# Kernel optimization log

Hardware: AMD Instinct MI355X
Metric: run time of the kernel (lower is better)

The kernel has to match this reference:

```python
import jax, jax.numpy as jnp
import numpy as np

N_HEAD = 16
SPARSE_TOPK = 64
NEG_INF = float('-inf')


def setup_inputs() -> dict:
    key = jax.random.key(0)
    ks = jax.random.split(key, 12)
    B, T, C = 4, 1024, 1024
    s = 0.02
    q = jax.random.normal(ks[0], (B, T, C), jnp.float32)
    kv = jax.random.normal(ks[1], (B, T, C), jnp.float32)  # forward asserts k == v
    tgt_mask = jnp.tril(jnp.ones((T, T), jnp.bool_)).reshape(1, 1, T, T)
    inp = {'q': q, 'k': kv, 'v': kv, 'tgt_mask': tgt_mask}
    for i, n in enumerate(['Wq', 'Wk', 'Wv', 'Wo']):
        inp[n] = jax.random.normal(ks[2 + i], (C, C), jnp.float32) * s
    for i, n in enumerate(['bq', 'bk', 'bv', 'bo']):
        inp[n] = jax.random.normal(ks[6 + i], (C,), jnp.float32) * s
    return inp


def reference(q, k, v, tgt_mask, Wq, Wk, Wv, Wo, bq, bk, bv, bo):
    B, T, C = q.shape
    H = N_HEAD
    hd = C // H
    scale = 1.0 / np.sqrt(hd).astype(np.float32)
    # QKV projections -> [B, H, T, hd]
    qh = (q @ Wq + bq).reshape(B, T, H, hd).transpose(0, 2, 1, 3)
    kh = (k @ Wk + bk).reshape(B, T, H, hd).transpose(0, 2, 1, 3)
    vh = (v @ Wv + bv).reshape(B, T, H, hd).transpose(0, 2, 1, 3)
    # full attention scores [B, H, T, T]
    att = jnp.einsum('bhtd,bhsd->bhts', qh, kh) * scale
    # causal mask: masked_fill where tgt_mask == 0
    att = jnp.where(tgt_mask[:, :, :T, :T], att, NEG_INF)
    # top-k sparse pruning: keep entries >= k-th largest per row (ties kept)
    top, _ = jax.lax.top_k(att, SPARSE_TOPK)
    vk = top[..., -1:]  # [B, H, T, 1]
    att = jnp.where(att < vk, NEG_INF, att)
    att = jax.nn.softmax(att, axis=-1)
    # dropout is identity in eval (p=0.0)
    y = jnp.einsum('bhts,bhsd->bhtd', att, vh)
    y = y.transpose(0, 2, 1, 3).reshape(B, T, C)
    return y @ Wo + bo
```

## Files before the change

### kernel.cpp

```cpp
#include <hip/hip_runtime.h>
#include <hip/hip_bf16.h>
#include <math.h>

typedef __attribute__((ext_vector_type(8))) short short8;
typedef __attribute__((ext_vector_type(4))) float f32x4;
typedef __attribute__((ext_vector_type(4))) int int4v;

#define SCL 0.1803368801111204f

static __device__ __forceinline__ unsigned short f2bf(float f) {
  unsigned u = __float_as_uint(f);
  u = u + 0x7FFFu + ((u >> 16) & 1u);
  return (unsigned short)(u >> 16);
}

static __device__ __forceinline__ unsigned keyof(float x) {
  unsigned u = __float_as_uint(x);
  return (u & 0x80000000u) ? ~u : (u | 0x80000000u);
}
static __device__ __forceinline__ float keyinv(unsigned k) {
  unsigned u = (k & 0x80000000u) ? (k & 0x7FFFFFFFu) : ~k;
  return __uint_as_float(u);
}

#define DPP_RED_STEP(x, OP, CTRL) \
  x = OP(x, __int_as_float(__builtin_amdgcn_mov_dpp(__float_as_int(x), CTRL, 0xf, 0xf, true)))
static __device__ __forceinline__ void red_maxmin(float& mx, float& mn) {
  DPP_RED_STEP(mx, fmaxf, 0xB1); DPP_RED_STEP(mn, fminf, 0xB1);
  DPP_RED_STEP(mx, fmaxf, 0x4E); DPP_RED_STEP(mn, fminf, 0x4E);
  DPP_RED_STEP(mx, fmaxf, 0x141); DPP_RED_STEP(mn, fminf, 0x141);
  DPP_RED_STEP(mx, fmaxf, 0x140); DPP_RED_STEP(mn, fminf, 0x140);
  mx = fmaxf(mx, __shfl_xor(mx, 16)); mn = fminf(mn, __shfl_xor(mn, 16));
  mx = fmaxf(mx, __shfl_xor(mx, 32)); mn = fminf(mn, __shfl_xor(mn, 32));
}
static __device__ __forceinline__ float red_sum(float s) {
  DPP_RED_STEP(s, __builtin_fmaf(1.f, 0.f, 0.f) + , 0);
  return s;
}
#undef DPP_RED_STEP
static __device__ __forceinline__ float red_sum2(float s) {
#define DPP_ADD(x, CTRL) \
  x = x + __int_as_float(__builtin_amdgcn_mov_dpp(__float_as_int(x), CTRL, 0xf, 0xf, true))
  DPP_ADD(s, 0xB1); DPP_ADD(s, 0x4E); DPP_ADD(s, 0x141); DPP_ADD(s, 0x140);
#undef DPP_ADD
  s += __shfl_xor(s, 16);
  s += __shfl_xor(s, 32);
  return s;
}

static __device__ __forceinline__ int saddr(int r, int cc) {
  return (((r << 9) + cc) << 2) ^ ((r & 7) << 4);
}
static __device__ __forceinline__ int paddr(int r, int c) {
  return ((r << 11) + (c << 1)) ^ ((r & 7) << 4);
}

static __device__ __forceinline__ void gld_lds16(const unsigned short* g, unsigned short* l) {
  __builtin_amdgcn_global_load_lds(
      (const __attribute__((address_space(1))) void*)g,
      (__attribute__((address_space(3))) void*)l, 16, 0, 0);
}

__global__ __launch_bounds__(256) void cvt3_k(const float* __restrict__ q,
                                              const float* __restrict__ k,
                                              const float* __restrict__ v,
                                              unsigned short* __restrict__ oq,
                                              unsigned short* __restrict__ ok,
                                              unsigned short* __restrict__ ov) {
  const int y = blockIdx.y;
  const float* in = (y == 0) ? q : (y == 1) ? k : v;
  unsigned short* out = (y == 0) ? oq : (y == 1) ? ok : ov;
  const int i = blockIdx.x * 256 + threadIdx.x;
  const f32x4* p = (const f32x4*)in + 2 * (size_t)i;
  f32x4 a = p[0], b = p[1];
  short8 r;
  r[0] = (short)f2bf(a[0]); r[1] = (short)f2bf(a[1]);
  r[2] = (short)f2bf(a[2]); r[3] = (short)f2bf(a[3]);
  r[4] = (short)f2bf(b[0]); r[5] = (short)f2bf(b[1]);
  r[6] = (short)f2bf(b[2]); r[7] = (short)f2bf(b[3]);
  ((short8*)out)[i] = r;
}

__global__ __launch_bounds__(256) void wtrans4_k(const float* __restrict__ Wq,
                                                 const float* __restrict__ Wk,
                                                 const float* __restrict__ Wv,
                                                 const float* __restrict__ Wo,
                                                 unsigned short* __restrict__ Wqt,
                                                 unsigned short* __restrict__ Wkt,
                                                 unsigned short* __restrict__ Wvt,
                                                 unsigned short* __restrict__ Wot) {
  const int z = blockIdx.z;
  const float* W = (z == 0) ? Wq : (z == 1) ? Wk : (z == 2) ? Wv : Wo;
  unsigned short* Wt = (z == 0) ? Wqt : (z == 1) ? Wkt : (z == 2) ? Wvt : Wot;
  __shared__ float tile[32][33];
  const int tx = threadIdx.x, ty = threadIdx.y;
  const int x0 = blockIdx.x * 32, y0 = blockIdx.y * 32;
#pragma unroll
  for (int j = 0; j < 4; ++j)
    tile[ty + j * 8][tx] = W[(y0 + ty + j * 8) * 1024 + x0 + tx];
  __syncthreads();
#pragma unroll
  for (int j = 0; j < 4; ++j)
    Wt[(x0 + ty + j * 8) * 1024 + (y0 + tx)] = f2bf(tile[tx][ty + j * 8]);
}

template <int MODE>
static __device__ __forceinline__ void gemm_body(unsigned short* As0, unsigned short* Bs0,
                                                 unsigned short* As1, unsigned short* Bs1,
                                                 const unsigned short* __restrict__ A,
                                                 const unsigned short* __restrict__ Bt,
                                                 const float* __restrict__ bias,
                                                 void* __restrict__ out) {
  const int tid = threadIdx.x;
  const int lane = tid & 63, w = tid >> 6;
  const int wr = w >> 1, wc = w & 1;
  const int m0 = blockIdx.y * 128, n0 = blockIdx.x * 128;
  const int l15 = lane & 15, l4 = lane >> 4;
  f32x4 acc[4][4] = {};
  const int r0 = tid >> 2, s0 = (tid & 3) * 8;
  const int r1 = r0 + 64;
  const unsigned short* gA0 = A + (m0 + r0) * 1024 + s0;
  const unsigned short* gA1 = A + (m0 + r1) * 1024 + s0;
  const unsigned short* gB0 = Bt + (n0 + r0) * 1024 + s0;
  const unsigned short* gB1 = Bt + (n0 + r1) * 1024 + s0;
  const int oA0 = r0 * 32 + s0, oA1 = r1 * 32 + s0;

  gld_lds16(gA0, As0 + oA0);
  gld_lds16(gA1, As0 + oA1);
  gld_lds16(gB0, Bs0 + oA0);
  gld_lds16(gB1, Bs0 + oA1);
  __syncthreads();

  for (int kt = 0; kt < 32; ++kt) {
    if (kt < 31) {
      const int k0n = (kt + 1) * 32;
      unsigned short* Asn = (kt & 1) ? As0 : As1;
      unsigned short* Bsn = (kt & 1) ? Bs0 : Bs1;
      gld_lds16(gA0 + k0n, Asn + oA0);
      gld_lds16(gA1 + k0n, Asn + oA1);
      gld_lds16(gB0 + k0n, Bsn + oA0);
      gld_lds16(gB1 + k0n, Bsn + oA1);
    }
    const unsigned short* Asc = (kt & 1) ? As1 : As0;
    const unsigned short* Bsc = (kt & 1) ? Bs1 : Bs0;
    short8 af[4], bfr[4];
#pragma unroll
    for (int i = 0; i < 4; ++i) {
      af[i]  = *(const short8*)(Asc + (wr * 64 + i * 16 + l15) * 32 + l4 * 8);
      bfr[i] = *(const short8*)(Bsc + (wc * 64 + i * 16 + l15) * 32 + l4 * 8);
    }
#pragma unroll
    for (int i = 0; i < 4; ++i)
#pragma unroll
      for (int j = 0; j < 4; ++j)
        acc[i][j] = __builtin_amdgcn_mfma_f32_16x16x32_bf16(af[i], bfr[j], acc[i][j], 0, 0, 0);
    __syncthreads();
  }
#pragma unroll
  for (int i = 0; i < 4; ++i) {
#pragma unroll
    for (int j = 0; j < 4; ++j) {
      const int n = n0 + wc * 64 + j * 16 + l15;
      const float bv = bias[n];
#pragma unroll
      for (int r = 0; r < 4; ++r) {
        const int m = m0 + wr * 64 + i * 16 + l4 * 4 + r;
        const float v = acc[i][j][r] + bv;
        if (MODE == 2) {
          ((float*)out)[m * 1024 + n] = v;
        } else {
          const int bb = m >> 10, t = m & 1023, hh = n >> 6, dd = n & 63;
          const unsigned short bfv = f2bf(v);
          if (MODE == 0)
            ((unsigned short*)out)[(((bb << 4) + hh) * 1024 + t) * 64 + dd] = bfv;
          else
            ((unsigned short*)out)[(((bb << 4) + hh) * 64 + dd) * 1024 + t] = bfv;
        }
      }
    }
  }
}

__global__ __launch_bounds__(256) void gemm_qkv_k(
    const unsigned short* qbf, const unsigned short* kbf, const unsigned short* vbf,
    const unsigned short* Wqt, const unsigned short* Wkt, const unsigned short* Wvt,
    const float* bq, const float* bk, const float* bv,
    unsigned short* Qh, unsigned short* Kh, unsigned short* Vth) {
  __shared__ unsigned short As0[128 * 32], Bs0[128 * 32], As1[128 * 32], Bs1[128 * 32];
  const int z = blockIdx.z;
  const unsigned short* A  = (z == 0) ? qbf : ((z == 1) ? kbf : vbf);
  const unsigned short* Bt = (z == 0) ? Wqt : ((z == 1) ? Wkt : Wvt);
  const float* bias        = (z == 0) ? bq  : ((z == 1) ? bk  : bv);
  if (z == 2) gemm_body<1>(As0, Bs0, As1, Bs1, A, Bt, bias, Vth);
  else        gemm_body<0>(As0, Bs0, As1, Bs1, A, Bt, bias, z ? Kh : Qh);
}

__global__ __launch_bounds__(256) void gemm_out_k(const unsigned short* Y,
                                                  const unsigned short* Wot,
                                                  const float* bo, float* out) {
  __shared__ unsigned short As0[128 * 32], Bs0[128 * 32], As1[128 * 32], Bs1[128 * 32];
  gemm_body<2>(As0, Bs0, As1, Bs1, Y, Wot, bo, out);
}

__global__ __launch_bounds__(1024, 8) void attn_k(const unsigned short* __restrict__ Q,
                                                  const unsigned short* __restrict__ K,
                                                  const unsigned short* __restrict__ Vt,
                                                  unsigned short* __restrict__ Y) {
  extern __shared__ __align__(16) char smem[];
  const int tid = threadIdx.x, lane = tid & 63, w = tid >> 6;
  const int t0 = 1008 - 16 * (int)blockIdx.x;
  const int h = blockIdx.y, b = blockIdx.z;
  const unsigned short* Qp = Q + (((b * 16 + h) * 1024) + t0) * 64;
  const unsigned short* Kh = K + (b * 16 + h) * 65536;
  const unsigned short* Vh = Vt + (b * 16 + h) * 65536;
  const int L = t0 + 16;
  const int Lpad = (L + 31) & ~31;
  const int nCT = L >> 4;
  const bool full = (L > 512);
  const int l15 = lane & 15, l4 = lane >> 4;
  float* RED3 = (float*)(smem + 32768);
  float* RED2 = (float*)(smem + 32768 + 13056);

  const short8 aq0 = *(const short8*)(Qp + l15 * 64 + l4 * 8);
  const short8 aq1 = *(const short8*)(Qp + l15 * 64 + 32 + l4 * 8);

  auto qk_tiles = [&](int tlo, int thi) {
    for (int ct = tlo + w; ct < thi; ct += 16) {
      const int c0 = ct * 16;
      const short8 kb0 = *(const short8*)(Kh + (c0 + l15) * 64 + l4 * 8);
      const short8 kb1 = *(const short8*)(Kh + (c0 + l15) * 64 + 32 + l4 * 8);
      f32x4 acc = {0.f, 0.f, 0.f, 0.f};
      acc = __builtin_amdgcn_mfma_f32_16x16x32_bf16(aq0, kb0, acc, 0, 0, 0);
      acc = __builtin_amdgcn_mfma_f32_16x16x32_bf16(aq1, kb1, acc, 0, 0, 0);
      const int c = c0 + l15, cc = c & 511;
      if (ct == nCT - 1) {
#pragma unroll
        for (int r = 0; r < 4; ++r) {
          const int row = l4 * 4 + r;
          *(float*)(smem + saddr(row, cc)) = (c <= t0 + row) ? acc[r] * SCL : -INFINITY;
        }
      } else {
#pragma unroll
        for (int r = 0; r < 4; ++r)
          *(float*)(smem + saddr(l4 * 4 + r, cc)) = acc[r] * SCL;
      }
    }
  };

  qk_tiles(0, full ? 32 : nCT);
  __syncthreads();

  const int Lr = t0 + w + 1;
  float v[16];
#pragma unroll
  for (int p = 0; p < 4; ++p) {
    const int c = (p << 7) + (lane << 1);
    const float2 t = *(const float2*)(smem + saddr(w, c));
    const bool vld = full || (c < L);
    v[2 * p]     = vld ? t.x : -INFINITY;
    v[2 * p + 1] = vld ? t.y : -INFINITY;
  }
  if (full) {
    __syncthreads();
    qk_tiles(32, nCT);
    __syncthreads();
#pragma unroll
    for (int p = 0; p < 4; ++p) {
      const int cc = (p << 7) + (lane << 1);
      const float2 t = *(const float2*)(smem + saddr(w, cc));
      const bool vld = (cc + 512) < L;
      v[8 + 2 * p] = vld ? t.x : -INFINITY;
      v[9 + 2 * p] = vld ? t.y : -INFINITY;
    }
  } else {
#pragma unroll
    for (int i = 8; i < 16; ++i) v[i] = -INFINITY;
  }

  float lm = v[0];
#pragma unroll
  for (int i = 1; i < 16; ++i) lm = fmaxf(lm, v[i]);
  float mx = lm, mn = lm;
  red_maxmin(mx, mn);

  auto countge = [&](float tm) {
    int cnt = 0;
#pragma unroll
    for (int i = 0; i < 8; ++i) cnt += (int)__popcll(__ballot(v[i] >= tm));
    if (full) {
#pragma unroll
      for (int i = 8; i < 16; ++i) cnt += (int)__popcll(__ballot(v[i] >= tm));
    }
    return cnt;
  };

  float thr = -INFINITY;
  if (Lr > 64) {
    unsigned lo = (unsigned)__builtin_amdgcn_readfirstlane((int)keyof(mn));
    unsigned hi = (unsigned)__builtin_amdgcn_readfirstlane((int)keyof(mx)) + 1u;
    int cl = Lr, ch = 0, alt = 0;
    for (int it = 0; it < 64 && (hi - lo) > 1u; ++it) {
      const unsigned span = hi - lo;
      unsigned off;
      if (alt) off = span >> 1;
      else {
        const float fr = (float)(cl - 64) / (float)(cl - ch);
        off = (unsigned)(fr * (float)span);
        if (off < 1u) off = 1u;
        if (off > span - 1u) off = span - 1u;
      }
      alt ^= 1;
      const unsigned mid = lo + off;
      const int cnt = countge(keyinv(mid));
      if (cnt >= 64) { lo = mid; cl = cnt; if (cnt == 64) hi = mid + 1u; }
      else { hi = mid; ch = cnt; }
    }
    thr = keyinv(lo);
  }

  float s = 0.f;
  unsigned pk[8];
#pragma unroll
  for (int p = 0; p < 4; ++p) {
    const float p0 = (v[2 * p]     >= thr) ? exp2f(v[2 * p]     - mx) : 0.f;
    const float p1 = (v[2 * p + 1] >= thr) ? exp2f(v[2 * p + 1] - mx) : 0.f;
    s += p0 + p1;
    pk[p] = (unsigned)f2bf(p0) | ((unsigned)f2bf(p1) << 16);
  }
  if (full) {
#pragma unroll
    for (int p = 4; p < 8; ++p) {
      const float p0 = (v[2 * p]     >= thr) ? exp2f(v[2 * p]     - mx) : 0.f;
      const float p1 = (v[2 * p + 1] >= thr) ? exp2f(v[2 * p + 1] - mx) : 0.f;
      s += p0 + p1;
      pk[p] = (unsigned)f2bf(p0) | ((unsigned)f2bf(p1) << 16);
    }
  }
#pragma unroll
  for (int p = 0; p < 4; ++p) {
    const int c = (p << 7) + (lane << 1);
    if (c < Lpad) *(unsigned*)(smem + paddr(w, c)) = pk[p];
  }
  if (full) {
#pragma unroll
    for (int p = 4; p < 8; ++p) {
      const int c = ((p & 3) << 7) + (lane << 1) + 512;
      if (c < Lpad) *(unsigned*)(smem + paddr(w, c)) = pk[p];
    }
  }
  s = red_sum2(s);
  if (lane == 0) RED2[w] = 1.f / s;
  __syncthreads();

  const int nST = Lpad >> 5;
  const int qd = (nST + 3) >> 2;
  const int kseg = w >> 2;
  const int d0 = (w & 3) * 16;
  int klo = kseg * qd, khi = klo + qd;
  if (klo > nST) klo = nST;
  if (khi > nST) khi = nST;
  f32x4 acc = {0.f, 0.f, 0.f, 0.f};
  for (int st = klo; st < khi; ++st) {
    const int sb = st * 32 + l4 * 8;
    const short8 paf = *(const short8*)(smem + paddr(l15, sb));
    const short8 vb = *(const short8*)(Vh + (d0 + l15) * 1024 + sb);
    acc = __builtin_amdgcn_mfma_f32_16x16x32_bf16(paf, vb, acc, 0, 0, 0);
  }
  if (kseg > 0) {
#pragma unroll
    for (int r = 0; r < 4; ++r)
      RED3[((kseg - 1) * 16 + l4 * 4 + r) * 68 + d0 + l15] = acc[r];
  }
  __syncthreads();
  if (kseg == 0) {
    const int d = (h << 6) + d0 + l15;
#pragma unroll
    for (int r = 0; r < 4; ++r) {
      const int row = l4 * 4 + r;
      const int col = d0 + l15;
      float sv = acc[r] + RED3[row * 68 + col] + RED3[(16 + row) * 68 + col] +
                 RED3[(32 + row) * 68 + col];
      Y[((b << 10) + t0 + row) * 1024 + d] = f2bf(sv * RED2[row]);
    }
  }
}

extern "C" void kernel_launch(void* const* d_in, const int* in_sizes, int n_in,
                              void* d_out, int out_size, void* d_ws, size_t ws_size,
                              hipStream_t stream) {
  const float* q  = (const float*)d_in[0];
  const float* k  = (const float*)d_in[1];
  const float* v  = (const float*)d_in[2];
  const float* Wq = (const float*)d_in[4];
  const float* Wk = (const float*)d_in[5];
  const float* Wv = (const float*)d_in[6];
  const float* Wo = (const float*)d_in[7];
  const float* bq = (const float*)d_in[8];
  const float* bk = (const float*)d_in[9];
  const float* bv = (const float*)d_in[10];
  const float* bo = (const float*)d_in[11];

  char* ws = (char*)d_ws;
  const size_t MB = 1u << 20;
  unsigned short* qbf = (unsigned short*)(ws + 0 * MB);
  unsigned short* kbf = (unsigned short*)(ws + 8 * MB);
  unsigned short* vbf = (unsigned short*)(ws + 16 * MB);
  unsigned short* Wqt = (unsigned short*)(ws + 24 * MB);
  unsigned short* Wkt = (unsigned short*)(ws + 26 * MB);
  unsigned short* Wvt = (unsigned short*)(ws + 28 * MB);
  unsigned short* Wot = (unsigned short*)(ws + 30 * MB);
  unsigned short* Qh  = (unsigned short*)(ws + 32 * MB);
  unsigned short* Kh  = (unsigned short*)(ws + 40 * MB);
  unsigned short* Vth = (unsigned short*)(ws + 48 * MB);
  unsigned short* Y   = qbf;

  cvt3_k<<<dim3(2048, 3), 256, 0, stream>>>(q, k, v, qbf, kbf, vbf);
  wtrans4_k<<<dim3(32, 32, 4), dim3(32, 8), 0, stream>>>(Wq, Wk, Wv, Wo, Wqt, Wkt, Wvt, Wot);
  gemm_qkv_k<<<dim3(8, 32, 3), 256, 0, stream>>>(qbf, kbf, vbf, Wqt, Wkt, Wvt,
                                                 bq, bk, bv, Qh, Kh, Vth);
  attn_k<<<dim3(64, 16, 4), 1024, 45888, stream>>>(Qh, Kh, Vth, Y);
  gemm_out_k<<<dim3(8, 32), 256, 0, stream>>>(Y, Wot, bo, (float*)d_out);
}
```

Measured before the change: 219.2 us.

## Store attention scores as fp16 in LDS and probe two thresholds per top-k search step

Scores are now written to shared memory as fp16 using the existing bf16 P-tile swizzled layout. This halves the score footprint, so all column tiles fit in one pass and the second QK pass and its two barriers are gone. The top-k threshold search now evaluates an interpolated split and a bisection split in each iteration, stops early on an exact count of 64, and caps the loop at 40 iterations. Rounding scores to fp16 can merge distinct values into ties and change which entries clear the threshold, so accuracy against the fp32 reference is at risk.

```diff
diff --git a/kernel.cpp b/kernel.cpp
--- a/kernel.cpp
+++ b/kernel.cpp
@@ -12,6 +12,12 @@
   unsigned u = __float_as_uint(f);
   u = u + 0x7FFFu + ((u >> 16) & 1u);
   return (unsigned short)(u >> 16);
+}
+static __device__ __forceinline__ unsigned short f2h(float f) {
+  return __builtin_bit_cast(unsigned short, (_Float16)f);
+}
+static __device__ __forceinline__ float h2f(unsigned short u) {
+  return (float)__builtin_bit_cast(_Float16, u);
 }
 
 static __device__ __forceinline__ unsigned keyof(float x) {
@@ -33,10 +39,6 @@
   mx = fmaxf(mx, __shfl_xor(mx, 16)); mn = fminf(mn, __shfl_xor(mn, 16));
   mx = fmaxf(mx, __shfl_xor(mx, 32)); mn = fminf(mn, __shfl_xor(mn, 32));
 }
-static __device__ __forceinline__ float red_sum(float s) {
-  DPP_RED_STEP(s, __builtin_fmaf(1.f, 0.f, 0.f) + , 0);
-  return s;
-}
 #undef DPP_RED_STEP
 static __device__ __forceinline__ float red_sum2(float s) {
 #define DPP_ADD(x, CTRL) \
@@ -48,9 +50,6 @@
   return s;
 }
 
-static __device__ __forceinline__ int saddr(int r, int cc) {
-  return (((r << 9) + cc) << 2) ^ ((r & 7) << 4);
-}
 static __device__ __forceinline__ int paddr(int r, int c) {
   return ((r << 11) + (c << 1)) ^ ((r & 7) << 4);
 }
@@ -224,30 +223,27 @@
   const short8 aq0 = *(const short8*)(Qp + l15 * 64 + l4 * 8);
   const short8 aq1 = *(const short8*)(Qp + l15 * 64 + 32 + l4 * 8);
 
-  auto qk_tiles = [&](int tlo, int thi) {
-    for (int ct = tlo + w; ct < thi; ct += 16) {
-      const int c0 = ct * 16;
-      const short8 kb0 = *(const short8*)(Kh + (c0 + l15) * 64 + l4 * 8);
-      const short8 kb1 = *(const short8*)(Kh + (c0 + l15) * 64 + 32 + l4 * 8);
-      f32x4 acc = {0.f, 0.f, 0.f, 0.f};
-      acc = __builtin_amdgcn_mfma_f32_16x16x32_bf16(aq0, kb0, acc, 0, 0, 0);
-      acc = __builtin_amdgcn_mfma_f32_16x16x32_bf16(aq1, kb1, acc, 0, 0, 0);
-      const int c = c0 + l15, cc = c & 511;
-      if (ct == nCT - 1) {
-#pragma unroll
-        for (int r = 0; r < 4; ++r) {
-          const int row = l4 * 4 + r;
-          *(float*)(smem + saddr(row, cc)) = (c <= t0 + row) ? acc[r] * SCL : -INFINITY;
-        }
-      } else {
-#pragma unroll
-        for (int r = 0; r < 4; ++r)
-          *(float*)(smem + saddr(l4 * 4 + r, cc)) = acc[r] * SCL;
+  for (int ct = w; ct < nCT; ct += 16) {
+    const int c0 = ct * 16;
+    const short8 kb0 = *(const short8*)(Kh + (c0 + l15) * 64 + l4 * 8);
+    const short8 kb1 = *(const short8*)(Kh + (c0 + l15) * 64 + 32 + l4 * 8);
+    f32x4 acc = {0.f, 0.f, 0.f, 0.f};
+    acc = __builtin_amdgcn_mfma_f32_16x16x32_bf16(aq0, kb0, acc, 0, 0, 0);
+    acc = __builtin_amdgcn_mfma_f32_16x16x32_bf16(aq1, kb1, acc, 0, 0, 0);
+    const int c = c0 + l15;
+    if (ct == nCT - 1) {
+#pragma unroll
+      for (int r = 0; r < 4; ++r) {
+        const int row = l4 * 4 + r;
+        *(unsigned short*)(smem + paddr(row, c)) =
+            (c <= t0 + row) ? f2h(acc[r] * SCL) : (unsigned short)0xFC00u;
       }
-    }
-  };
-
-  qk_tiles(0, full ? 32 : nCT);
+    } else {
+#pragma unroll
+      for (int r = 0; r < 4; ++r)
+        *(unsigned short*)(smem + paddr(l4 * 4 + r, c)) = f2h(acc[r] * SCL);
+    }
+  }
   __syncthreads();
 
   const int Lr = t0 + w + 1;
@@ -255,22 +251,19 @@
 #pragma unroll
   for (int p = 0; p < 4; ++p) {
     const int c = (p << 7) + (lane << 1);
-    const float2 t = *(const float2*)(smem + saddr(w, c));
+    const unsigned u = *(const unsigned*)(smem + paddr(w, c));
     const bool vld = full || (c < L);
-    v[2 * p]     = vld ? t.x : -INFINITY;
-    v[2 * p + 1] = vld ? t.y : -INFINITY;
+    v[2 * p]     = vld ? h2f((unsigned short)(u & 0xFFFFu)) : -INFINITY;
+    v[2 * p + 1] = vld ? h2f((unsigned short)(u >> 16)) : -INFINITY;
   }
   if (full) {
-    __syncthreads();
-    qk_tiles(32, nCT);
-    __syncthreads();
 #pragma unroll
     for (int p = 0; p < 4; ++p) {
-      const int cc = (p << 7) + (lane << 1);
-      const float2 t = *(const float2*)(smem + saddr(w, cc));
-      const bool vld = (cc + 512) < L;
-      v[8 + 2 * p] = vld ? t.x : -INFINITY;
-      v[9 + 2 * p] = vld ? t.y : -INFINITY;
+      const int c = (p << 7) + (lane << 1) + 512;
+      const unsigned u = *(const unsigned*)(smem + paddr(w, c));
+      const bool vld = c < L;
+      v[8 + 2 * p] = vld ? h2f((unsigned short)(u & 0xFFFFu)) : -INFINITY;
+      v[9 + 2 * p] = vld ? h2f((unsigned short)(u >> 16)) : -INFINITY;
     }
   } else {
 #pragma unroll
@@ -298,22 +291,28 @@
   if (Lr > 64) {
     unsigned lo = (unsigned)__builtin_amdgcn_readfirstlane((int)keyof(mn));
     unsigned hi = (unsigned)__builtin_amdgcn_readfirstlane((int)keyof(mx)) + 1u;
-    int cl = Lr, ch = 0, alt = 0;
-    for (int it = 0; it < 64 && (hi - lo) > 1u; ++it) {
+    int cl = Lr, ch = 0;
+    for (int it = 0; it < 40 && (hi - lo) > 1u; ++it) {
       const unsigned span = hi - lo;
-      unsigned off;
-      if (alt) off = span >> 1;
-      else {
-        const float fr = (float)(cl - 64) / (float)(cl - ch);
-        off = (unsigned)(fr * (float)span);
-        if (off < 1u) off = 1u;
-        if (off > span - 1u) off = span - 1u;
+      const float fr = (float)(cl - 64) / (float)(cl - ch);
+      unsigned offS = (unsigned)(fr * (float)span);
+      if (offS < 1u) offS = 1u;
+      if (offS > span - 1u) offS = span - 1u;
+      unsigned k1 = lo + offS;
+      unsigned k2 = lo + (span >> 1);
+      if (k2 < 1u + lo) k2 = lo + 1u;
+      if (k1 > k2) { const unsigned t = k1; k1 = k2; k2 = t; }
+      const int c1 = countge(keyinv(k1));
+      const int c2 = countge(keyinv(k2));
+      if (c2 >= 64) {
+        lo = k2; cl = c2;
+        if (c2 == 64) break;
+      } else if (c1 >= 64) {
+        lo = k1; cl = c1; hi = k2; ch = c2;
+        if (c1 == 64) break;
+      } else {
+        hi = k1; ch = c1;
       }
-      alt ^= 1;
-      const unsigned mid = lo + off;
-      const int cnt = countge(keyinv(mid));
-      if (cnt >= 64) { lo = mid; cl = cnt; if (cnt == 64) hi = mid + 1u; }
-      else { hi = mid; ch = cnt; }
     }
     thr = keyinv(lo);
   }
```

After: 252.8 us. 15.3% more time.
